# Optimization experiments

Hardware: AMD Instinct MI355X
Metric: run time of the kernel (lower is better)

Reference implementation:

```python
import jax, jax.numpy as jnp
import numpy as np
from jax import lax

T, D, L, K = 8192, 1024, 2, 2
ALPHA = 0.1  # reservoir leak rate


def setup_inputs() -> dict:
    key = jax.random.key(0)
    ks = jax.random.split(key, 6)
    s = 1.0 / np.sqrt(D)  # keep recurrence stable
    return {
        "x_seq": jax.random.normal(ks[0], (T, D), jnp.float32),
        "Wx": jax.random.normal(ks[1], (L, D, D), jnp.float32) * s,
        "Wh": jax.random.normal(ks[2], (L, D, D), jnp.float32) * s,
        "Wr": jax.random.normal(ks[3], (L, K, D, D), jnp.float32) * s,
        "U": jax.random.normal(ks[4], (L, K, D, D), jnp.float32) * s,
        "b": jnp.zeros((L, D), jnp.float32),
    }


def _layer(x_seq, Wx, Wh, Wr, U, b):
    # one CRSD layer: scan the recurrent cell over time, state kept in carry
    def step(carry, x_t):
        h, r = carry  # h: [D], r: [K, D]
        pre = Wx @ x_t + Wh @ h + jnp.einsum("kij,kj->i", Wr, r) + b
        h_new = jnp.tanh(pre)
        r_new = (1.0 - ALPHA) * r + ALPHA * jnp.tanh(jnp.einsum("kij,j->ki", U, h_new))
        return (h_new, r_new), h_new

    init = (jnp.zeros((D,), x_seq.dtype), jnp.zeros((K, D), x_seq.dtype))
    _, out_seq = lax.scan(step, init, x_seq)
    return out_seq  # [T, D]


def reference(x_seq, Wx, Wh, Wr, U, b):
    # stacked layers: output sequence of layer l feeds layer l+1
    for l in range(L):
        x_seq = _layer(x_seq, Wx[l], Wh[l], Wr[l], U[l], b[l])
    return x_seq  # [T, D]
```

## Files before the change

kernel.cpp:

```cpp
#include <hip/hip_runtime.h>
#include <math.h>

#define TT 8192
#define DD 1024
#define LWG 64
#define NWG 128
#define TPB 512
#define GCAP (1 << 15)

typedef __attribute__((ext_vector_type(2))) float f32x2;
typedef __attribute__((ext_vector_type(4))) float f32x4;

__device__ __forceinline__ void vdrain() { asm volatile("s_waitcnt vmcnt(0)" ::: "memory"); }
__device__ __forceinline__ void st4_x(float* p, f32x4 v) {
  asm volatile("global_store_dwordx4 %0, %1, off sc0 sc1" :: "v"(p), "v"(v) : "memory");
}
__device__ __forceinline__ void stu_x(unsigned* p, unsigned v) {
  asm volatile("global_store_dword %0, %1, off sc0 sc1" :: "v"(p), "v"(v) : "memory");
}
__device__ __forceinline__ f32x4 ld4_x(const float* p) {
  f32x4 r;
  asm volatile("global_load_dwordx4 %0, %1, off sc0 sc1\n\ts_waitcnt vmcnt(0)"
               : "=&v"(r) : "v"(p) : "memory");
  return r;
}
__device__ __forceinline__ void ld4_x2(const float* p0, const float* p1, f32x4& a, f32x4& b) {
  asm volatile("global_load_dwordx4 %0, %2, off sc0 sc1\n\t"
               "global_load_dwordx4 %1, %3, off sc0 sc1\n\t"
               "s_waitcnt vmcnt(0)"
               : "=&v"(a), "=&v"(b) : "v"(p0), "v"(p1) : "memory");
}
__device__ __forceinline__ unsigned ldu_x(const unsigned* p) {
  unsigned r;
  asm volatile("global_load_dword %0, %1, off sc0 sc1\n\ts_waitcnt vmcnt(0)"
               : "=&v"(r) : "v"(p) : "memory");
  return r;
}

__device__ __forceinline__ f32x4 pollep(const float* p, float epf, unsigned* abortf) {
  int g = 0;
  for (;;) {
    f32x4 v = ld4_x(p);
    if (v.z == epf) return v;
    if ((++g & 255) == 0) {
      if (ldu_x(abortf)) return v;
      if (g > GCAP) { stu_x(abortf, 1u); vdrain(); return v; }
    }
    if (g & 2) __builtin_amdgcn_s_sleep(1);
  }
}
__device__ __forceinline__ void pollep2(const float* p0, const float* p1, float epf,
                                        unsigned* abortf, f32x4& a, f32x4& b) {
  int g = 0;
  for (;;) {
    ld4_x2(p0, p1, a, b);
    if (a.z == epf && b.z == epf) return;
    if ((++g & 255) == 0) {
      if (ldu_x(abortf)) return;
      if (g > GCAP) { stu_x(abortf, 1u); vdrain(); return; }
    }
    if (g & 2) __builtin_amdgcn_s_sleep(1);
  }
}

#define HT_FLOATS (2 * 8 * 512 * 4)
#define RT_FLOATS (2 * 2 * 2 * 512 * 4)
__global__ void init_arena(float* __restrict__ arena, unsigned* __restrict__ tg) {
  const int idx = blockIdx.x * 256 + threadIdx.x;
  if (idx < HT_FLOATS + RT_FLOATS) arena[idx] = 0.f;
  if (idx < 2048) tg[idx] = 0u;
}

__global__ __launch_bounds__(TPB, 1)
void crsd_seq(const float* __restrict__ pwx, const float* __restrict__ Wx,
              const float* __restrict__ Wh, const float* __restrict__ Wr,
              const float* __restrict__ Uw, const float* __restrict__ bias,
              float* __restrict__ out, float* __restrict__ arena,
              unsigned* __restrict__ tg) {
  const int wg = blockIdx.x, tid = threadIdx.x;
  const int wv = tid >> 6, ln = tid & 63;
  const int layer = wg >> 6, g = wg & 63;
  const int rb = g * 16 + 2 * wv;
  const size_t MS = (size_t)DD * DD;

  float* hT0 = arena;
  float* hTL = arena + (size_t)layer * 8 * 512 * 4;
  float* rT  = arena + HT_FLOATS;
  unsigned* stamp = tg;
  unsigned* abortf = tg + 1024;

  __shared__ __align__(16) float sh_x[DD];
  __shared__ __align__(16) float sh_h[DD];
  __shared__ __align__(16) float sh_r[2 * DD];

  const float* Whp = Wh + (size_t)layer * MS;
  const float* Wrp = Wr + (size_t)layer * 2 * MS;
  const float* Up  = Uw + (size_t)layer * 2 * MS;

  float wh[2][16], wr[2][2][16], wx[2][16], uw[2][2][16];
#pragma unroll
  for (int ri = 0; ri < 2; ++ri) {
    const int row = rb + ri;
#pragma unroll
    for (int c = 0; c < 4; ++c) {
      const int j = 4 * ln + 256 * c;
      f32x4 a = *(const f32x4*)&Whp[(size_t)row * DD + j];
      wh[ri][4*c+0]=a.x; wh[ri][4*c+1]=a.y; wh[ri][4*c+2]=a.z; wh[ri][4*c+3]=a.w;
      f32x4 b0 = *(const f32x4*)&Wrp[(size_t)row * DD + j];
      wr[ri][0][4*c+0]=b0.x; wr[ri][0][4*c+1]=b0.y; wr[ri][0][4*c+2]=b0.z; wr[ri][0][4*c+3]=b0.w;
      f32x4 b1 = *(const f32x4*)&Wrp[MS + (size_t)row * DD + j];
      wr[ri][1][4*c+0]=b1.x; wr[ri][1][4*c+1]=b1.y; wr[ri][1][4*c+2]=b1.z; wr[ri][1][4*c+3]=b1.w;
      if (layer) {
        f32x4 xw = *(const f32x4*)&Wx[MS + (size_t)row * DD + j];
        wx[ri][4*c+0]=xw.x; wx[ri][4*c+1]=xw.y; wx[ri][4*c+2]=xw.z; wx[ri][4*c+3]=xw.w;
      } else {
        wx[ri][4*c+0]=0.f; wx[ri][4*c+1]=0.f; wx[ri][4*c+2]=0.f; wx[ri][4*c+3]=0.f;
      }
      f32x4 u0 = *(const f32x4*)&Up[(size_t)row * DD + j];
      uw[0][ri][4*c+0]=u0.x; uw[0][ri][4*c+1]=u0.y; uw[0][ri][4*c+2]=u0.z; uw[0][ri][4*c+3]=u0.w;
      f32x4 u1 = *(const f32x4*)&Up[MS + (size_t)row * DD + j];
      uw[1][ri][4*c+0]=u1.x; uw[1][ri][4*c+1]=u1.y; uw[1][ri][4*c+2]=u1.z; uw[1][ri][4*c+3]=u1.w;
    }
  }
  float bb0 = 0.f, bb1 = 0.f;
  if (layer) { bb0 = bias[DD + rb]; bb1 = bias[DD + rb + 1]; }
  float rown[2][2] = {{0.f, 0.f}, {0.f, 0.f}};
  sh_h[tid] = 0.f;
  sh_h[tid + 512] = 0.f;

  for (int t = 0; t < TT; ++t) {
    const int cu = t & 7;
    const float eph = (float)(t + 1);

    if (t > 0) {
      const float epr = (float)t;
      const int ps = (t - 1) & 1;
      f32x4 ra, rc;
      pollep2(rT + ((((size_t)(layer * 2 + 0) * 2 + ps) * 512) + tid) * 4,
              rT + ((((size_t)(layer * 2 + 1) * 2 + ps) * 512) + tid) * 4,
              epr, abortf, ra, rc);
      f32x2 w0; w0.x = ra.x; w0.y = ra.y;
      f32x2 w1; w1.x = rc.x; w1.y = rc.y;
      *(f32x2*)&sh_r[2 * tid] = w0;
      *(f32x2*)&sh_r[1024 + 2 * tid] = w1;
    } else {
      sh_r[2 * tid] = 0.f; sh_r[2 * tid + 1] = 0.f;
      sh_r[1024 + 2 * tid] = 0.f; sh_r[1024 + 2 * tid + 1] = 0.f;
    }
    if (layer) {
      f32x4 xv = pollep(hT0 + ((size_t)cu * 512 + tid) * 4, eph, abortf);
      f32x2 wxv; wxv.x = xv.x; wxv.y = xv.y;
      *(f32x2*)&sh_x[2 * tid] = wxv;
    } else if (wv == 0 && t >= 8) {
      const unsigned tgt = (unsigned)(t - 7);
      const unsigned* sp = stamp + (ln << 4);
      int gg = 0;
      for (;;) {
        const unsigned v = ldu_x(sp);
        if (__all((int)(v >= tgt))) break;
        if ((++gg & 255) == 0) {
          if (ldu_x(abortf)) break;
          if (gg > GCAP) { stu_x(abortf, 1u); vdrain(); break; }
        }
        __builtin_amdgcn_s_sleep(1);
      }
    }
    float pw0 = 0.f, pw1 = 0.f;
    if (!layer && ln == 0) {
      const f32x2 p2 = *(const f32x2*)&pwx[(size_t)t * DD + rb];
      pw0 = p2.x; pw1 = p2.y;
    }
    __syncthreads();
    if (layer && tid == 0) stu_x(stamp + (g << 4), (unsigned)(t + 1));

    float acc0 = 0.f, acc1 = 0.f;
#pragma unroll
    for (int c = 0; c < 4; ++c) {
      const int j = 4 * ln + 256 * c;
      const f32x4 hv = *(const f32x4*)&sh_h[j];
      const f32x4 r0 = *(const f32x4*)&sh_r[j];
      const f32x4 r1v = *(const f32x4*)&sh_r[DD + j];
      acc0 += wh[0][4*c+0]*hv.x + wh[0][4*c+1]*hv.y + wh[0][4*c+2]*hv.z + wh[0][4*c+3]*hv.w
            + wr[0][0][4*c+0]*r0.x + wr[0][0][4*c+1]*r0.y + wr[0][0][4*c+2]*r0.z + wr[0][0][4*c+3]*r0.w
            + wr[0][1][4*c+0]*r1v.x + wr[0][1][4*c+1]*r1v.y + wr[0][1][4*c+2]*r1v.z + wr[0][1][4*c+3]*r1v.w;
      acc1 += wh[1][4*c+0]*hv.x + wh[1][4*c+1]*hv.y + wh[1][4*c+2]*hv.z + wh[1][4*c+3]*hv.w
            + wr[1][0][4*c+0]*r0.x + wr[1][0][4*c+1]*r0.y + wr[1][0][4*c+2]*r0.z + wr[1][0][4*c+3]*r0.w
            + wr[1][1][4*c+0]*r1v.x + wr[1][1][4*c+1]*r1v.y + wr[1][1][4*c+2]*r1v.z + wr[1][1][4*c+3]*r1v.w;
      if (layer) {
        const f32x4 xv = *(const f32x4*)&sh_x[j];
        acc0 += wx[0][4*c+0]*xv.x + wx[0][4*c+1]*xv.y + wx[0][4*c+2]*xv.z + wx[0][4*c+3]*xv.w;
        acc1 += wx[1][4*c+0]*xv.x + wx[1][4*c+1]*xv.y + wx[1][4*c+2]*xv.z + wx[1][4*c+3]*xv.w;
      }
    }
#pragma unroll
    for (int off = 32; off; off >>= 1) {
      acc0 += __shfl_xor(acc0, off, 64);
      acc1 += __shfl_xor(acc1, off, 64);
    }
    if (ln == 0) {
      f32x4 ht;
      ht.x = tanhf(acc0 + (layer ? bb0 : pw0));
      ht.y = tanhf(acc1 + (layer ? bb1 : pw1));
      ht.z = eph; ht.w = 0.f;
      st4_x(hTL + ((size_t)cu * 512 + g * 8 + wv) * 4, ht);
      if (layer) {
        f32x2 ov; ov.x = ht.x; ov.y = ht.y;
        *(f32x2*)&out[(size_t)t * DD + rb] = ov;
      }
    }
    if (t == TT - 1) break;
    __syncthreads();

    {
      f32x4 hv4 = pollep(hTL + ((size_t)cu * 512 + tid) * 4, eph, abortf);
      f32x2 wh2; wh2.x = hv4.x; wh2.y = hv4.y;
      *(f32x2*)&sh_h[2 * tid] = wh2;
    }
    __syncthreads();

    float ua[2][2];
#pragma unroll
    for (int k = 0; k < 2; ++k)
#pragma unroll
      for (int ri = 0; ri < 2; ++ri) {
        float a = 0.f;
#pragma unroll
        for (int c = 0; c < 4; ++c) {
          const int j = 4 * ln + 256 * c;
          const f32x4 hv = *(const f32x4*)&sh_h[j];
          a += uw[k][ri][4*c+0]*hv.x + uw[k][ri][4*c+1]*hv.y
             + uw[k][ri][4*c+2]*hv.z + uw[k][ri][4*c+3]*hv.w;
        }
#pragma unroll
        for (int off = 32; off; off >>= 1) a += __shfl_xor(a, off, 64);
        ua[k][ri] = a;
      }
    if (ln == 0) {
      const int ps = t & 1;
#pragma unroll
      for (int k = 0; k < 2; ++k) {
        rown[k][0] = 0.9f * rown[k][0] + 0.1f * tanhf(ua[k][0]);
        rown[k][1] = 0.9f * rown[k][1] + 0.1f * tanhf(ua[k][1]);
        f32x4 rt;
        rt.x = rown[k][0]; rt.y = rown[k][1]; rt.z = eph; rt.w = 0.f;
        st4_x(rT + ((((size_t)(layer * 2 + k) * 2 + ps) * 512) + g * 8 + wv) * 4, rt);
      }
    }
  }
}

__global__ __launch_bounds__(256)
void gemm_bias(const float* __restrict__ A, const float* __restrict__ W,
               const float* __restrict__ bias, float* __restrict__ C) {
  __shared__ float As[32][65];
  __shared__ float Ws[32][65];
  const int tid = threadIdx.x;
  const int bm = blockIdx.x * 64;
  const int bn = blockIdx.y * 64;
  const int ty = tid >> 4, tx = tid & 15;
  float acc[4][4] = {};
  for (int k0 = 0; k0 < DD; k0 += 32) {
#pragma unroll
    for (int p = 0; p < 2; ++p) {
      const int idx = tid + p * 256;
      const int r = idx >> 3;
      const int cf = idx & 7;
      float4 av = *(const float4*)&A[(size_t)(bm + r) * DD + k0 + cf * 4];
      As[cf*4+0][r] = av.x; As[cf*4+1][r] = av.y; As[cf*4+2][r] = av.z; As[cf*4+3][r] = av.w;
      float4 wv = *(const float4*)&W[(size_t)(bn + r) * DD + k0 + cf * 4];
      Ws[cf*4+0][r] = wv.x; Ws[cf*4+1][r] = wv.y; Ws[cf*4+2][r] = wv.z; Ws[cf*4+3][r] = wv.w;
    }
    __syncthreads();
#pragma unroll
    for (int kk = 0; kk < 32; ++kk) {
      float a[4], w[4];
#pragma unroll
      for (int e = 0; e < 4; ++e) { a[e] = As[kk][ty * 4 + e]; w[e] = Ws[kk][tx * 4 + e]; }
#pragma unroll
      for (int i = 0; i < 4; ++i)
#pragma unroll
        for (int j = 0; j < 4; ++j) acc[i][j] += a[i] * w[j];
    }
    __syncthreads();
  }
#pragma unroll
  for (int i = 0; i < 4; ++i) {
    const int m = bm + ty * 4 + i;
#pragma unroll
    for (int j = 0; j < 4; ++j) {
      const int n = bn + tx * 4 + j;
      C[(size_t)m * DD + n] = acc[i][j] + bias[n];
    }
  }
}

extern "C" void kernel_launch(void* const* d_in, const int* in_sizes, int n_in,
                              void* d_out, int out_size, void* d_ws, size_t ws_size,
                              hipStream_t stream) {
  const float* x  = (const float*)d_in[0];
  const float* Wx = (const float*)d_in[1];
  const float* Wh = (const float*)d_in[2];
  const float* Wr = (const float*)d_in[3];
  const float* U  = (const float*)d_in[4];
  const float* b  = (const float*)d_in[5];
  float* out = (float*)d_out;

  float* pwx = (float*)d_ws;
  float* arena = pwx + (size_t)TT * DD;
  unsigned* tg = (unsigned*)(arena + HT_FLOATS + RT_FLOATS);

  hipLaunchKernelGGL(init_arena, dim3(192), dim3(256), 0, stream, arena, tg);
  hipLaunchKernelGGL(gemm_bias, dim3(TT / 64, DD / 64), dim3(256), 0, stream,
                     x, Wx, b, pwx);

  const float* pwxc = pwx;
  float* arenap = arena;
  unsigned* tgp = tg;
  void* args[] = { (void*)&pwxc, (void*)&Wx, (void*)&Wh, (void*)&Wr,
                   (void*)&U, (void*)&b, (void*)&out, (void*)&arenap, (void*)&tgp };
  hipLaunchCooperativeKernel((const void*)crsd_seq, dim3(NWG), dim3(TPB),
                             args, 0, stream);
}
```

Before: 34.70 ms.

## Precompute Wh·h after r publish, merge polls, drop barrier, tune spin backoff

Moves the Wh·h partial product out of the critical path. It is now computed right after r is published, using the h already in shared memory, so the next step only adds the Wr·r and Wx·x terms after its poll completes. For layer 1 the r and x polls are merged into one three-load poll, and one __syncthreads before the h poll is removed. Spin loops now busy-poll for 16 tries before sleeping, which cuts wake-up latency but adds memory traffic and risks a shared-memory race if the removed barrier was protecting reuse of sh_h.

```diff
diff --git a/kernel.cpp b/kernel.cpp
--- a/kernel.cpp
+++ b/kernel.cpp
@@ -30,6 +30,14 @@
                "s_waitcnt vmcnt(0)"
                : "=&v"(a), "=&v"(b) : "v"(p0), "v"(p1) : "memory");
 }
+__device__ __forceinline__ void ld4_x3(const float* p0, const float* p1, const float* p2,
+                                       f32x4& a, f32x4& b, f32x4& c) {
+  asm volatile("global_load_dwordx4 %0, %3, off sc0 sc1\n\t"
+               "global_load_dwordx4 %1, %4, off sc0 sc1\n\t"
+               "global_load_dwordx4 %2, %5, off sc0 sc1\n\t"
+               "s_waitcnt vmcnt(0)"
+               : "=&v"(a), "=&v"(b), "=&v"(c) : "v"(p0), "v"(p1), "v"(p2) : "memory");
+}
 __device__ __forceinline__ unsigned ldu_x(const unsigned* p) {
   unsigned r;
   asm volatile("global_load_dword %0, %1, off sc0 sc1\n\ts_waitcnt vmcnt(0)"
@@ -42,11 +50,13 @@
   for (;;) {
     f32x4 v = ld4_x(p);
     if (v.z == epf) return v;
-    if ((++g & 255) == 0) {
-      if (ldu_x(abortf)) return v;
-      if (g > GCAP) { stu_x(abortf, 1u); vdrain(); return v; }
-    }
-    if (g & 2) __builtin_amdgcn_s_sleep(1);
+    if (++g > 16) {
+      if ((g & 255) == 0) {
+        if (ldu_x(abortf)) return v;
+        if (g > GCAP) { stu_x(abortf, 1u); vdrain(); return v; }
+      }
+      __builtin_amdgcn_s_sleep(2);
+    }
   }
 }
 __device__ __forceinline__ void pollep2(const float* p0, const float* p1, float epf,
@@ -55,11 +65,29 @@
   for (;;) {
     ld4_x2(p0, p1, a, b);
     if (a.z == epf && b.z == epf) return;
-    if ((++g & 255) == 0) {
-      if (ldu_x(abortf)) return;
-      if (g > GCAP) { stu_x(abortf, 1u); vdrain(); return; }
-    }
-    if (g & 2) __builtin_amdgcn_s_sleep(1);
+    if (++g > 16) {
+      if ((g & 255) == 0) {
+        if (ldu_x(abortf)) return;
+        if (g > GCAP) { stu_x(abortf, 1u); vdrain(); return; }
+      }
+      __builtin_amdgcn_s_sleep(2);
+    }
+  }
+}
+__device__ __forceinline__ void pollep3(const float* p0, const float* p1, const float* p2,
+                                        float epr, float eph, unsigned* abortf,
+                                        f32x4& a, f32x4& b, f32x4& c) {
+  int g = 0;
+  for (;;) {
+    ld4_x3(p0, p1, p2, a, b, c);
+    if (a.z == epr && b.z == epr && c.z == eph) return;
+    if (++g > 16) {
+      if ((g & 255) == 0) {
+        if (ldu_x(abortf)) return;
+        if (g > GCAP) { stu_x(abortf, 1u); vdrain(); return; }
+      }
+      __builtin_amdgcn_s_sleep(2);
+    }
   }
 }
 
@@ -125,8 +153,7 @@
   float bb0 = 0.f, bb1 = 0.f;
   if (layer) { bb0 = bias[DD + rb]; bb1 = bias[DD + rb + 1]; }
   float rown[2][2] = {{0.f, 0.f}, {0.f, 0.f}};
-  sh_h[tid] = 0.f;
-  sh_h[tid + 512] = 0.f;
+  float wp0 = 0.f, wp1 = 0.f;
 
   for (int t = 0; t < TT; ++t) {
     const int cu = t & 7;
@@ -135,10 +162,17 @@
     if (t > 0) {
       const float epr = (float)t;
       const int ps = (t - 1) & 1;
+      const float* rp0 = rT + ((((size_t)(layer * 2 + 0) * 2 + ps) * 512) + tid) * 4;
+      const float* rp1 = rT + ((((size_t)(layer * 2 + 1) * 2 + ps) * 512) + tid) * 4;
       f32x4 ra, rc;
-      pollep2(rT + ((((size_t)(layer * 2 + 0) * 2 + ps) * 512) + tid) * 4,
-              rT + ((((size_t)(layer * 2 + 1) * 2 + ps) * 512) + tid) * 4,
-              epr, abortf, ra, rc);
+      if (layer) {
+        f32x4 xv;
+        pollep3(rp0, rp1, hT0 + ((size_t)cu * 512 + tid) * 4, epr, eph, abortf, ra, rc, xv);
+        f32x2 wxv; wxv.x = xv.x; wxv.y = xv.y;
+        *(f32x2*)&sh_x[2 * tid] = wxv;
+      } else {
+        pollep2(rp0, rp1, epr, abortf, ra, rc);
+      }
       f32x2 w0; w0.x = ra.x; w0.y = ra.y;
       f32x2 w1; w1.x = rc.x; w1.y = rc.y;
       *(f32x2*)&sh_r[2 * tid] = w0;
@@ -146,23 +180,26 @@
     } else {
       sh_r[2 * tid] = 0.f; sh_r[2 * tid + 1] = 0.f;
       sh_r[1024 + 2 * tid] = 0.f; sh_r[1024 + 2 * tid + 1] = 0.f;
-    }
-    if (layer) {
-      f32x4 xv = pollep(hT0 + ((size_t)cu * 512 + tid) * 4, eph, abortf);
-      f32x2 wxv; wxv.x = xv.x; wxv.y = xv.y;
-      *(f32x2*)&sh_x[2 * tid] = wxv;
-    } else if (wv == 0 && t >= 8) {
+      if (layer) {
+        f32x4 xv = pollep(hT0 + ((size_t)cu * 512 + tid) * 4, eph, abortf);
+        f32x2 wxv; wxv.x = xv.x; wxv.y = xv.y;
+        *(f32x2*)&sh_x[2 * tid] = wxv;
+      }
+    }
+    if (!layer && wv == 0 && t >= 8) {
       const unsigned tgt = (unsigned)(t - 7);
       const unsigned* sp = stamp + (ln << 4);
       int gg = 0;
       for (;;) {
         const unsigned v = ldu_x(sp);
         if (__all((int)(v >= tgt))) break;
-        if ((++gg & 255) == 0) {
-          if (ldu_x(abortf)) break;
-          if (gg > GCAP) { stu_x(abortf, 1u); vdrain(); break; }
+        if (++gg > 16) {
+          if ((gg & 255) == 0) {
+            if (ldu_x(abortf)) break;
+            if (gg > GCAP) { stu_x(abortf, 1u); vdrain(); break; }
+          }
+          __builtin_amdgcn_s_sleep(2);
         }
-        __builtin_amdgcn_s_sleep(1);
       }
     }
     float pw0 = 0.f, pw1 = 0.f;
@@ -173,18 +210,15 @@
     __syncthreads();
     if (layer && tid == 0) stu_x(stamp + (g << 4), (unsigned)(t + 1));
 
-    float acc0 = 0.f, acc1 = 0.f;
+    float acc0 = wp0, acc1 = wp1;
 #pragma unroll
     for (int c = 0; c < 4; ++c) {
       const int j = 4 * ln + 256 * c;
-      const f32x4 hv = *(const f32x4*)&sh_h[j];
       const f32x4 r0 = *(const f32x4*)&sh_r[j];
       const f32x4 r1v = *(const f32x4*)&sh_r[DD + j];
-      acc0 += wh[0][4*c+0]*hv.x + wh[0][4*c+1]*hv.y + wh[0][4*c+2]*hv.z + wh[0][4*c+3]*hv.w
-            + wr[0][0][4*c+0]*r0.x + wr[0][0][4*c+1]*r0.y + wr[0][0][4*c+2]*r0.z + wr[0][0][4*c+3]*r0.w
+      acc0 += wr[0][0][4*c+0]*r0.x + wr[0][0][4*c+1]*r0.y + wr[0][0][4*c+2]*r0.z + wr[0][0][4*c+3]*r0.w
             + wr[0][1][4*c+0]*r1v.x + wr[0][1][4*c+1]*r1v.y + wr[0][1][4*c+2]*r1v.z + wr[0][1][4*c+3]*r1v.w;
-      acc1 += wh[1][4*c+0]*hv.x + wh[1][4*c+1]*hv.y + wh[1][4*c+2]*hv.z + wh[1][4*c+3]*hv.w
-            + wr[1][0][4*c+0]*r0.x + wr[1][0][4*c+1]*r0.y + wr[1][0][4*c+2]*r0.z + wr[1][0][4*c+3]*r0.w
+      acc1 += wr[1][0][4*c+0]*r0.x + wr[1][0][4*c+1]*r0.y + wr[1][0][4*c+2]*r0.z + wr[1][0][4*c+3]*r0.w
             + wr[1][1][4*c+0]*r1v.x + wr[1][1][4*c+1]*r1v.y + wr[1][1][4*c+2]*r1v.z + wr[1][1][4*c+3]*r1v.w;
       if (layer) {
         const f32x4 xv = *(const f32x4*)&sh_x[j];
@@ -209,7 +243,6 @@
       }
     }
     if (t == TT - 1) break;
-    __syncthreads();
 
     {
       f32x4 hv4 = pollep(hTL + ((size_t)cu * 512 + tid) * 4, eph, abortf);
@@ -245,6 +278,15 @@
         rt.x = rown[k][0]; rt.y = rown[k][1]; rt.z = eph; rt.w = 0.f;
         st4_x(rT + ((((size_t)(layer * 2 + k) * 2 + ps) * 512) + g * 8 + wv) * 4, rt);
       }
+    }
+
+    wp0 = 0.f; wp1 = 0.f;
+#pragma unroll
+    for (int c = 0; c < 4; ++c) {
+      const int j = 4 * ln + 256 * c;
+      const f32x4 hv = *(const f32x4*)&sh_h[j];
+      wp0 += wh[0][4*c+0]*hv.x + wh[0][4*c+1]*hv.y + wh[0][4*c+2]*hv.z + wh[0][4*c+3]*hv.w;
+      wp1 += wh[1][4*c+0]*hv.x + wh[1][4*c+1]*hv.y + wh[1][4*c+2]*hv.z + wh[1][4*c+3]*hv.w;
     }
   }
 }
```

Result: slower. 40.85 ms (+17.7%).
